# Kernel optimization log

Measured on AMD Instinct MI355X. Metric: run time of the kernel, lower is better.

The kernel has to match this reference:

```python
import jax, jax.numpy as jnp
import numpy as np

jax.config.update("jax_enable_x64", True)

B, N, M_EQ, D_INEQ = 64, 128, 32, 64
RHO = 1.0
THRES = 1e-5
MAX_ITERS = 5000  # safety cap (original loops until relative objective change <= 1e-5)


def setup_inputs() -> dict:
    key = jax.random.key(0)
    kL, kq, kG, kA, kx0, ks = jax.random.split(key, 6)
    L = jax.random.normal(kL, (B, N, N))
    Q = jnp.einsum('bij,bkj->bik', L, L) / N + jnp.eye(N)  # SPD, well-conditioned
    q = jax.random.normal(kq, (B, N))
    G = jax.random.normal(kG, (B, D_INEQ, N))
    A = jax.random.normal(kA, (B, M_EQ, N))
    x0 = jax.random.normal(kx0, (B, N))
    slack = jax.random.uniform(ks, (B, D_INEQ)) + 0.1
    h = jnp.einsum('bdn,bn->bd', G, x0) + slack  # strictly feasible ineq
    b = jnp.einsum('bmn,bn->bm', A, x0)          # feasible eq
    f32 = jnp.float32
    return {"Q": Q.astype(f32), "q": q.astype(f32), "G": G.astype(f32),
            "h": h.astype(f32), "A": A.astype(f32), "b": b.astype(f32)}


def _alt_diff_batch(Q, q, G, h, A, b):
    """Batched Alt-Diff ADMM QP solve; returns (x [B,n], dx/dq [B,n,n])."""
    Bb, n = q.shape
    d = h.shape[1]
    m = b.shape[1]
    dt = Q.dtype
    AtA = jnp.einsum('bmi,bmj->bij', A, A)
    GtG = jnp.einsum('bdi,bdj->bij', G, G)
    R = -jnp.linalg.inv(Q + RHO * AtA + RHO * GtG)
    ATb = RHO * jnp.einsum('bmn,bm->bn', A, b)
    GTh = RHO * jnp.einsum('bdn,bd->bn', G, h)
    eye = jnp.eye(n, dtype=dt)

    def obj(x):
        return 0.5 * jnp.einsum('bi,bij,bj->b', x, Q, x) + jnp.einsum('bi,bi->b', q, x)

    init = dict(
        xk=jnp.zeros((Bb, n), dt), sk=jnp.zeros((Bb, d), dt),
        lamb=jnp.zeros((Bb, m), dt), nu=jnp.zeros((Bb, d), dt),
        dxk=jnp.zeros((Bb, n, n), dt), dsk=jnp.zeros((Bb, d, n), dt),
        dlamb=jnp.zeros((Bb, m, n), dt), dnu=jnp.zeros((Bb, d, n), dt),
        res_prev=jnp.full((Bb,), 1000.0, dt),   # res = [1000, -100] init
        res_cur=jnp.full((Bb,), -100.0, dt),
        done=jnp.zeros((Bb,), bool),
        it=jnp.zeros((), jnp.int32),
    )

    def cond(s):
        return jnp.logical_and(jnp.any(~s["done"]), s["it"] < MAX_ITERS)

    def body(s):
        xk = jnp.einsum('bij,bj->bi', R,
                        q + jnp.einsum('bmn,bm->bn', A, s["lamb"])
                          + jnp.einsum('bdn,bd->bn', G, s["nu"]) - ATb
                          + RHO * jnp.einsum('bdn,bd->bn', G, s["sk"]) - GTh)
        dxk = jnp.einsum('bij,bjk->bik', R,
                         eye + jnp.einsum('bmn,bmk->bnk', A, s["dlamb"])
                             + jnp.einsum('bdn,bdk->bnk', G, s["dnu"])
                             + RHO * jnp.einsum('bdn,bdk->bnk', G, s["dsk"]))
        Gx = jnp.einsum('bdn,bn->bd', G, xk)
        sk = jax.nn.relu(-(1.0 / RHO) * s["nu"] - (Gx - h))
        sgn = (sk > 0).astype(dt)  # sgn applied to already-relu'd sk, as in source
        dsk = (-1.0 / RHO) * sgn[:, :, None] * (s["dnu"] + RHO * jnp.einsum('bdn,bnk->bdk', G, dxk))
        lamb = s["lamb"] + RHO * (jnp.einsum('bmn,bn->bm', A, xk) - b)
        dlamb = s["dlamb"] + RHO * jnp.einsum('bmn,bnk->bmk', A, dxk)
        nu = s["nu"] + RHO * (Gx + sk - h)
        dnu = s["dnu"] + RHO * (jnp.einsum('bdn,bnk->bdk', G, dxk) + dsk)
        res_new = obj(xk)

        keep = s["done"]

        def sel(old, new):
            mask = keep.reshape((-1,) + (1,) * (new.ndim - 1))
            return jnp.where(mask, old, new)

        res_prev = jnp.where(keep, s["res_prev"], s["res_cur"])
        res_cur = jnp.where(keep, s["res_cur"], res_new)
        done = keep | (jnp.abs((res_cur - res_prev) / res_prev) <= THRES)
        return dict(
            xk=sel(s["xk"], xk), sk=sel(s["sk"], sk),
            lamb=sel(s["lamb"], lamb), nu=sel(s["nu"], nu),
            dxk=sel(s["dxk"], dxk), dsk=sel(s["dsk"], dsk),
            dlamb=sel(s["dlamb"], dlamb), dnu=sel(s["dnu"], dnu),
            res_prev=res_prev, res_cur=res_cur, done=done, it=s["it"] + 1,
        )

    final = jax.lax.while_loop(cond, body, init)
    return final["xk"], final["dxk"]


def reference(Q, q, G, h, A, b):
    out_dtype = q.dtype
    f64 = jnp.float64
    x, _dx = _alt_diff_batch(Q.astype(f64), q.astype(f64), G.astype(f64),
                             h.astype(f64), A.astype(f64), b.astype(f64))
    return x.astype(out_dtype)
```

## Files before the change

kernel.cpp:

```cpp
#include <hip/hip_runtime.h>

#define NN 128
#define ME 32
#define DI 64
#define NZ 96
#define ROWD 130
#define MAXIT 5000

#define OFF_UN 16640
#define ROWB  (OFF_UN)
#define COLB  (OFF_UN + 256)
#define PPK   (OFF_UN)
#define ZEXL  (OFF_UN + 384)
#define ZEXH  (OFF_UN + 512)
#define TVX   (OFF_UN + 576)
#define TV16  (OFF_UN + 704)
#define FLG   (OFF_UN + 736)
#define YBUF  (OFF_UN)
#define KBUF  (OFF_UN + 1536)
#define CPART (OFF_UN + 1024)
#define VP    (OFF_UN + 1280)
#define BASEV (OFF_UN + 1792)
#define QBV   (OFF_UN + 1888)
#define FPART (OFF_UN + 1024)
#define RHSV  (OFF_UN + 1280)
#define XPART (OFF_UN + 1408)
#define CB    (OFF_UN + 2688)
#define QBUF  (OFF_UN + 2816)
#define V1    (OFF_UN + 2944)
#define V2    (OFF_UN + 3072)
#define HB    (OFF_UN + 3200)
#define BB    (OFF_UN + 3264)
#define CST   (OFF_UN + 3296)
#define ZBF   (OFF_UN + 3304)
#define LDS_DBL (OFF_UN + 3400)

typedef __attribute__((ext_vector_type(2))) float f32x2;

__device__ __forceinline__ float rlf(float v, int lane) {
  return __uint_as_float((unsigned)__builtin_amdgcn_readlane((int)__float_as_uint(v), lane));
}
__device__ __forceinline__ f32x2 fma2(f32x2 a, f32x2 b, f32x2 c) {
  return __builtin_elementwise_fma(a, b, c);
}

#define MV2(PA, ZS, L0) {                                                  \
    f32x2 z0 = { rlf(ZS, L0), rlf(ZS, (L0)+1) };                           \
    A0 = fma2(Kp[PA], z0, A0); B0 = fma2(Kp2[PA], z0, B0);                 \
    f32x2 z1 = { rlf(ZS, (L0)+2), rlf(ZS, (L0)+3) };                       \
    A1 = fma2(Kp[(PA)+1], z1, A1); B1 = fma2(Kp2[(PA)+1], z1, B1); }

#define CPYRANGE(LBASE, KBASE, CNT)                                        \
  _Pragma("unroll") for (int j = 0; j < (CNT); ++j) {                      \
    const int lj = (LBASE) + j, kc = (KBASE) + j;                          \
    float va = (float)ldsd[KBUF + kc*NZ + l];                              \
    float vb = (float)ldsd[KBUF + kc*NZ + 64 + lm];                        \
    if ((lj & 1) == 0) { Kp[lj>>1].x = va; Kp2[lj>>1].x = vb; }            \
    else               { Kp[lj>>1].y = va; Kp2[lj>>1].y = vb; }            \
  }

__global__ __launch_bounds__(256, 1) void altdiff_kernel(
    const float* __restrict__ Qg, const float* __restrict__ qg,
    const float* __restrict__ Gg, const float* __restrict__ hg,
    const float* __restrict__ Ag, const float* __restrict__ bg,
    float* __restrict__ out)
{
  extern __shared__ double ldsd[];

  const int bidx = blockIdx.x;
  const int tid  = threadIdx.x;
  const int w    = tid >> 6;
  const int l    = tid & 63;
  const int lm   = l & 31;
  const int ia   = tid & 127;
  const int hh   = tid >> 7;

  const float* Qb = Qg + (size_t)bidx * NN * NN;
  const float* Ab = Ag + (size_t)bidx * ME * NN;
  const float* Gb = Gg + (size_t)bidx * DI * NN;
  const float* qb = qg + (size_t)bidx * NN;
  const float* hb = hg + (size_t)bidx * DI;
  const float* bv = bg + (size_t)bidx * ME;

  if (tid < DI) ldsd[HB + tid] = (double)hb[tid];
  else if (tid < DI + ME) ldsd[BB + tid - DI] = (double)bv[tid - DI];
  if (tid >= 128) ldsd[QBUF + tid - 128] = (double)qb[tid - 128];

  const int r = tid >> 4, c = tid & 15;
  double acc[8][8];

  {
    const float4* Q4 = (const float4*)Qb;
#pragma unroll
    for (int rr = 0; rr < 8; ++rr) {
      float4 q0 = Q4[((8*r+rr) << 5) + 2*c];
      float4 q1 = Q4[((8*r+rr) << 5) + 2*c + 1];
      acc[rr][0]=(double)q0.x; acc[rr][1]=(double)q0.y; acc[rr][2]=(double)q0.z; acc[rr][3]=(double)q0.w;
      acc[rr][4]=(double)q1.x; acc[rr][5]=(double)q1.y; acc[rr][6]=(double)q1.z; acc[rr][7]=(double)q1.w;
    }
    const float4* A4 = (const float4*)Ab;
    for (int m = 0; m < ME; ++m) {
      float4 u0 = A4[(m << 5) + 2*r], u1 = A4[(m << 5) + 2*r + 1];
      float4 v0 = A4[(m << 5) + 2*c], v1 = A4[(m << 5) + 2*c + 1];
      double uu[8] = {(double)u0.x,(double)u0.y,(double)u0.z,(double)u0.w,
                      (double)u1.x,(double)u1.y,(double)u1.z,(double)u1.w};
      double vv[8] = {(double)v0.x,(double)v0.y,(double)v0.z,(double)v0.w,
                      (double)v1.x,(double)v1.y,(double)v1.z,(double)v1.w};
#pragma unroll
      for (int rr = 0; rr < 8; ++rr)
#pragma unroll
        for (int cc = 0; cc < 8; ++cc)
          acc[rr][cc] = fma(uu[rr], vv[cc], acc[rr][cc]);
    }
    const float4* G4 = (const float4*)Gb;
    for (int d = 0; d < DI; ++d) {
      float4 u0 = G4[(d << 5) + 2*r], u1 = G4[(d << 5) + 2*r + 1];
      float4 v0 = G4[(d << 5) + 2*c], v1 = G4[(d << 5) + 2*c + 1];
      double uu[8] = {(double)u0.x,(double)u0.y,(double)u0.z,(double)u0.w,
                      (double)u1.x,(double)u1.y,(double)u1.z,(double)u1.w};
      double vv[8] = {(double)v0.x,(double)v0.y,(double)v0.z,(double)v0.w,
                      (double)v1.x,(double)v1.y,(double)v1.z,(double)v1.w};
#pragma unroll
      for (int rr = 0; rr < 8; ++rr)
#pragma unroll
        for (int cc = 0; cc < 8; ++cc)
          acc[rr][cc] = fma(uu[rr], vv[cc], acc[rr][cc]);
    }
  }

  {
    if (r == 0) {
#pragma unroll
      for (int cc = 0; cc < 8; ++cc) ldsd[ROWB + 8*c + cc] = acc[0][cc];
    }
    if (c == 0) {
#pragma unroll
      for (int rr = 0; rr < 8; ++rr) ldsd[COLB + 8*r + rr] = acc[rr][0];
    }
    __syncthreads();
    for (int k = 0; k < NN; ++k) {
      const int pb = (k & 1) << 7;
      const int krt = k >> 3, kcl = k & 7;
      double rowk[8], colv[8];
#pragma unroll
      for (int cc = 0; cc < 8; ++cc) rowk[cc] = ldsd[ROWB + pb + 8*c + cc];
#pragma unroll
      for (int rr = 0; rr < 8; ++rr) colv[rr] = ldsd[COLB + pb + 8*r + rr];
      const double dkk  = ldsd[ROWB + pb + k];
      const double rcpd = 1.0 / dkk;
      double rdv[8];
#pragma unroll
      for (int cc = 0; cc < 8; ++cc) rdv[cc] = rowk[cc] * rcpd;
      const bool pivR = (r == krt), pivC = (c == krt);
#pragma unroll
      for (int rr = 0; rr < 8; ++rr) {
        const double cv = colv[rr] * rcpd;
        const bool pr = pivR && (rr == kcl);
#pragma unroll
        for (int cc = 0; cc < 8; ++cc) {
          double gen = fma(-cv, rowk[cc], acc[rr][cc]);
          acc[rr][cc] = pr ? rdv[cc] : gen;
        }
      }
      if (pivC) {
#pragma unroll
        for (int cc = 0; cc < 8; ++cc) if (cc == kcl) {
#pragma unroll
          for (int rr = 0; rr < 8; ++rr) {
            const bool pr2 = pivR && (rr == kcl);
            acc[rr][cc] = pr2 ? -rcpd : colv[rr] * rcpd;
          }
        }
      }
      if (k < NN - 1) {
        const int pb2 = ((k + 1) & 1) << 7;
        const int krt2 = (k + 1) >> 3, kcl2 = (k + 1) & 7;
        if (r == krt2) {
#pragma unroll
          for (int rr = 0; rr < 8; ++rr) if (rr == kcl2) {
#pragma unroll
            for (int cc = 0; cc < 8; ++cc) ldsd[ROWB + pb2 + 8*c + cc] = acc[rr][cc];
          }
        }
        if (c == krt2) {
#pragma unroll
          for (int cc = 0; cc < 8; ++cc) if (cc == kcl2) {
#pragma unroll
            for (int rr = 0; rr < 8; ++rr) ldsd[COLB + pb2 + 8*r + rr] = acc[rr][cc];
          }
        }
      }
      __syncthreads();
    }
#pragma unroll
    for (int rr = 0; rr < 8; ++rr) {
      double2* dst = (double2*)(ldsd + (8*r+rr)*ROWD + 8*c);
#pragma unroll
      for (int t = 0; t < 4; ++t) dst[t] = make_double2(acc[rr][2*t], acc[rr][2*t+1]);
    }
  }
  __syncthreads();

  f32x2 Kp[16], Kp2[16];
  for (int blk = 0; blk < 8; ++blk) {
    {
      const float* gp[6];
#pragma unroll
      for (int jj = 0; jj < 6; ++jj) {
        int it = 12*blk + 6*hh + jj;
        gp[jj] = (it < DI) ? (Gb + it*NN) : (Ab + (it - DI)*NN);
      }
      double a2[6] = {0,0,0,0,0,0};
#pragma unroll 4
      for (int t = 0; t < NN; ++t) {
        double rv = ldsd[t*ROWD + ia];
#pragma unroll
        for (int jj = 0; jj < 6; ++jj)
          a2[jj] = fma(rv, (double)gp[jj][t], a2[jj]);
      }
      double2* yst = (double2*)(ldsd + YBUF + ia*12 + 6*hh);
#pragma unroll
      for (int p = 0; p < 3; ++p) yst[p] = make_double2(a2[2*p], a2[2*p+1]);
    }
    __syncthreads();
    {
      const int r2 = (ia < NZ) ? ia : 0;
      const float* brow = (r2 < DI) ? (Gb + r2*NN) : (Ab + (r2 - DI)*NN);
      double a2[6] = {0,0,0,0,0,0};
#pragma unroll 4
      for (int t = 0; t < NN; ++t) {
        double bvv = (double)brow[t];
        const double2* yr = (const double2*)(ldsd + YBUF + t*12 + 6*hh);
        double2 y0 = yr[0], y1 = yr[1], y2 = yr[2];
        a2[0] = fma(bvv, y0.x, a2[0]); a2[1] = fma(bvv, y0.y, a2[1]);
        a2[2] = fma(bvv, y1.x, a2[2]); a2[3] = fma(bvv, y1.y, a2[3]);
        a2[4] = fma(bvv, y2.x, a2[4]); a2[5] = fma(bvv, y2.y, a2[5]);
      }
      if (ia < NZ) {
#pragma unroll
        for (int jj = 0; jj < 6; ++jj) ldsd[KBUF + (6*hh + jj)*NZ + ia] = a2[jj];
      }
    }
    __syncthreads();
    if (w == 0) {
      if (blk == 0)      { CPYRANGE(0,  0, 12) }
      else if (blk == 1) { CPYRANGE(12, 0, 12) }
      else if (blk == 2) { CPYRANGE(24, 0, 8) }
    } else if (w == 1) {
      if (blk == 2)      { CPYRANGE(0,  8, 4) }
      else if (blk == 3) { CPYRANGE(4,  0, 12) }
      else if (blk == 4) { CPYRANGE(16, 0, 12) }
      else if (blk == 5) { CPYRANGE(28, 0, 4) }
    } else if (w == 2) {
      if (blk == 5)      { CPYRANGE(0,  4, 8) }
      else if (blk == 6) { CPYRANGE(8,  0, 12) }
      else if (blk == 7) { CPYRANGE(20, 0, 12) }
    }
    __syncthreads();
  }

  {
    double s = 0;
#pragma unroll 8
    for (int jc = 0; jc < 48; ++jc) {
      int j = 48*hh + jc;
      double coef = (j < DI) ? ldsd[HB + j] : ldsd[BB + j - DI];
      const float* src = (j < DI) ? (Gb + j*NN) : (Ab + (j - DI)*NN);
      s = fma(-(double)src[ia], coef, s);
    }
    ldsd[CPART + hh*128 + ia] = s;
  }
  __syncthreads();
  if (tid < NN) ldsd[CB + tid] = ldsd[QBUF + tid] + ldsd[CPART + tid] + ldsd[CPART + 128 + tid];
  __syncthreads();

  {
    double a = 0, b2 = 0;
#pragma unroll 4
    for (int tt = 0; tt < 64; ++tt) {
      int t = 64*hh + tt;
      double rv = ldsd[t*ROWD + ia];
      a  = fma(rv, ldsd[CB + t], a);
      b2 = fma(rv, ldsd[QBUF + t], b2);
    }
    ldsd[VP + hh*128 + ia] = a;
    ldsd[VP + 256 + hh*128 + ia] = b2;
  }
  __syncthreads();
  if (tid < NN) {
    ldsd[V1 + tid] = ldsd[VP + tid] + ldsd[VP + 128 + tid];
    ldsd[V2 + tid] = ldsd[VP + 256 + tid] + ldsd[VP + 384 + tid];
  }
  __syncthreads();

  {
    const int r2 = (ia < NZ) ? ia : 0;
    const float* brow = (r2 < DI) ? (Gb + r2*NN) : (Ab + (r2 - DI)*NN);
    const int voff = hh ? V2 : V1;
    double s = 0;
#pragma unroll 4
    for (int t = 0; t < NN; ++t) s = fma((double)brow[t], ldsd[voff + t], s);
    if (ia < NZ) ldsd[(hh ? QBV : BASEV) + ia] = s;
  }
  if (w == 0) {
    double pc = ldsd[V1+l]*ldsd[CB+l]   + ldsd[V1+64+l]*ldsd[CB+64+l];
    double pq = ldsd[V1+l]*ldsd[QBUF+l] + ldsd[V1+64+l]*ldsd[QBUF+64+l];
#pragma unroll
    for (int off = 32; off >= 1; off >>= 1) { pc += __shfl_xor(pc, off); pq += __shfl_xor(pq, off); }
    if (l == 0) { ldsd[CST] = pc; ldsd[CST+1] = pq; }
  }
  __syncthreads();

  const double baseA = ldsd[BASEV + l];
  const double baseB = ldsd[BASEV + 64 + lm];
  const double qvA   = ldsd[QBV + l];
  const double qvB   = ldsd[QBV + 64 + lm];
  const double hb2   = ldsd[HB + l] - baseA;
  const double bb2   = baseB - ldsd[BB + lm];
  const double S_uc  = ldsd[CST], S_qu = ldsd[CST + 1];
  double hnb = hb2, lb = bb2;
  double zlo = 0.0, zhi = 0.0;
  double zAlo = 0.0, zAhi = 0.0, zBlo = 0.0, zBhi = 0.0, zClo = 0.0, zChi = 0.0;
  double res_prev = 1000.0, res_cur = -100.0;
  float2 own = make_float2(0.f, 0.f);

  {
    if (w < 3) *(float2*)&ldsd[PPK + w*64 + l] = make_float2(0.f, 0.f);
    if (w == 0) ldsd[ZEXL + 64 + l] = 0.0;
    if (w == 2 && l < 32) ldsd[ZEXH + 32 + l] = 0.0;
    if (tid == 0) { ldsd[FLG] = 0.0; ldsd[FLG + 1] = 0.0; }
  }

  for (int it = 0; it < MAXIT + 3; ++it) {
    __syncthreads();
    const int buf = it & 1, nbuf = buf ^ 1;
    const int bprev = nbuf;
    const double fl = ldsd[FLG + bprev];
    const float2* pb = (const float2*)(ldsd + PPK + buf*192);

    if (w == 0) {
      float2 s1v = pb[64 + l], s2v = pb[128 + l];
      float slo = (own.x + s1v.x) + s2v.x;
      double t = hnb - (double)slo;
      float zflo = (float)fabs(t);
      if (it >= 3 && fl != 0.0) break;
      zClo = zBlo; zBlo = zAlo; zAlo = zlo;
      if (it < MAXIT) {
        zlo = fabs(t);
        ldsd[ZEXL + buf*64 + l] = zlo;
        hnb = hb2 + fmin(t, 0.0);
        f32x2 A0 = {0.f, 0.f}, A1 = A0, B0 = A0, B1 = A0;
        MV2(0,  zflo, 0)  MV2(2,  zflo, 4)  MV2(4,  zflo, 8)  MV2(6,  zflo, 12)
        MV2(8,  zflo, 16) MV2(10, zflo, 20) MV2(12, zflo, 24) MV2(14, zflo, 28)
        f32x2 As = A0 + A1, Bs = B0 + B1;
        float2 np = make_float2(As.x + As.y, Bs.x + Bs.y);
        *(float2*)&ldsd[PPK + nbuf*192 + l] = np;
        own = np;
      }
    } else if (w == 1) {
      float2 s0v = pb[l], s2v = pb[128 + l];
      float slo = (s0v.x + own.x) + s2v.x;
      double t = hnb - (double)slo;
      float zflo = (float)fabs(t);
      if (it >= 3 && fl != 0.0) break;
      if (it < MAXIT) {
        hnb = hb2 + fmin(t, 0.0);
        f32x2 A0 = {0.f, 0.f}, A1 = A0, B0 = A0, B1 = A0;
        MV2(0,  zflo, 32) MV2(2,  zflo, 36) MV2(4,  zflo, 40) MV2(6,  zflo, 44)
        MV2(8,  zflo, 48) MV2(10, zflo, 52) MV2(12, zflo, 56) MV2(14, zflo, 60)
        f32x2 As = A0 + A1, Bs = B0 + B1;
        float2 np = make_float2(As.x + As.y, Bs.x + Bs.y);
        *(float2*)&ldsd[PPK + nbuf*192 + 64 + l] = np;
        own = np;
      }
    } else if (w == 2) {
      float2 s0v = pb[l], s1v = pb[64 + l];
      float shi = (s0v.y + s1v.y) + own.y;
      double lamn = lb + (double)shi;
      float zfhi = (float)lamn;
      if (it >= 3 && fl != 0.0) break;
      zChi = zBhi; zBhi = zAhi; zAhi = zhi;
      if (it < MAXIT) {
        zhi = lamn;
        lb = lamn + bb2;
        if (l < 32) ldsd[ZEXH + buf*32 + l] = lamn;
        f32x2 A0 = {0.f, 0.f}, A1 = A0, B0 = A0, B1 = A0;
        MV2(0,  zfhi, 0)  MV2(2,  zfhi, 4)  MV2(4,  zfhi, 8)  MV2(6,  zfhi, 12)
        MV2(8,  zfhi, 16) MV2(10, zfhi, 20) MV2(12, zfhi, 24) MV2(14, zfhi, 28)
        f32x2 As = A0 + A1, Bs = B0 + B1;
        float2 np = make_float2(As.x + As.y, Bs.x + Bs.y);
        *(float2*)&ldsd[PPK + nbuf*192 + 128 + l] = np;
        own = np;
      }
    } else {
      float2 v0 = pb[l], v1 = pb[64 + l], v2 = pb[128 + l];
      const double zAl = ldsd[ZEXL + bprev*64 + l];
      const double zAh = ldsd[ZEXH + bprev*32 + lm];
      const int g = l & 15;
      const double* tq = ldsd + TVX + bprev*64;
      double a0 = tq[g], a1 = tq[g + 16], a2 = tq[g + 32], a3 = tq[g + 48];
      double t1v[16];
      const double2* tp = (const double2*)(ldsd + TV16 + bprev*16);
#pragma unroll
      for (int u = 0; u < 8; ++u) { double2 vv = tp[u]; t1v[2*u] = vv.x; t1v[2*u+1] = vv.y; }
      if (it >= 3 && fl != 0.0) break;
      if (it < MAXIT) {
        float slo_f = (v0.x + v1.x) + v2.x;
        float shi_f = (v0.y + v1.y) + v2.y;
        double yf  = (double)slo_f + baseA;
        double tvl = fma(qvA, zAl, -0.5*(zAl*(baseA + yf) + yf*yf));
        double yfB = (double)shi_f + baseB;
        double tvh = fma(qvB, zAh, -0.5*(zAh*(baseB + yfB) + yfB*yfB));
        ldsd[TVX + buf*64 + l] = tvl + ((l < 32) ? tvh : 0.0);
      }
      if (l < 16 && it >= 1 && it <= MAXIT)
        ldsd[TV16 + buf*16 + l] = (a0 + a1) + (a2 + a3);
      if (it >= 2 && it <= MAXIT + 1) {
        double s1 = ((t1v[0] + t1v[1]) + (t1v[2] + t1v[3])) + ((t1v[4] + t1v[5]) + (t1v[6] + t1v[7]));
        double s2 = ((t1v[8] + t1v[9]) + (t1v[10] + t1v[11])) + ((t1v[12] + t1v[13]) + (t1v[14] + t1v[15]));
        double obj = (s1 + s2) - 0.5*S_uc + S_qu;
        res_prev = res_cur; res_cur = obj;
        if (l == 0)
          ldsd[FLG + buf] = (fabs(res_cur - res_prev) <= 1e-5 * fabs(res_prev)) ? 1.0 : 0.0;
      }
    }
  }

  if (w == 0) ldsd[ZBF + l] = zClo;
  if (w == 2 && l < 32) ldsd[ZBF + 64 + l] = zChi;
  __syncthreads();
  {
    double s = 0;
#pragma unroll 8
    for (int jc = 0; jc < 48; ++jc) {
      int j = 48*hh + jc;
      double zj = ldsd[ZBF + j];
      const float* src = (j < DI) ? (Gb + j*NN) : (Ab + (j - DI)*NN);
      s = fma((double)src[ia], zj, s);
    }
    ldsd[FPART + hh*128 + ia] = s;
  }
  __syncthreads();
  if (tid < NN) ldsd[RHSV + tid] = ldsd[CB + tid] + ldsd[FPART + tid] + ldsd[FPART + 128 + tid];
  __syncthreads();
  {
    double s = 0;
#pragma unroll 4
    for (int tt = 0; tt < 64; ++tt) {
      int t = 64*hh + tt;
      s = fma(ldsd[t*ROWD + ia], ldsd[RHSV + t], s);
    }
    ldsd[XPART + hh*128 + ia] = s;
  }
  __syncthreads();
  if (tid < NN)
    out[(size_t)bidx * NN + tid] = (float)(ldsd[XPART + tid] + ldsd[XPART + 128 + tid]);
}

extern "C" void kernel_launch(void* const* d_in, const int* in_sizes, int n_in,
                              void* d_out, int out_size, void* d_ws, size_t ws_size,
                              hipStream_t stream) {
  (void)in_sizes; (void)n_in; (void)out_size; (void)d_ws; (void)ws_size;
  const float* Q = (const float*)d_in[0];
  const float* q = (const float*)d_in[1];
  const float* G = (const float*)d_in[2];
  const float* h = (const float*)d_in[3];
  const float* A = (const float*)d_in[4];
  const float* b = (const float*)d_in[5];
  float* out = (float*)d_out;
  const size_t lds_bytes = (size_t)LDS_DBL * sizeof(double);
  altdiff_kernel<<<dim3(64), dim3(256), lds_bytes, stream>>>(Q, q, G, h, A, b, out);
}
```

Baseline: 598.7 us.

## Spread ADMM matvec across all four waves and track iterates in float

Rebalances the per-iteration ADMM matvec so all four wavefronts each own 28/28/24/16 rows of the packed K matrix, rather than three waves doing the matvec while the fourth only evaluates the objective. Each wave now reads all four partial-sum slots and redundantly recomputes the z/lambda update, which removes the ZEXL/ZEXH exchange buffers. The history of iterates is kept in float instead of double. This shortens the matvec on the critical path per iteration, but adds an extra partial to read and sum, and the float history could change the convergence check and the final reconstruction.

```diff
diff --git a/kernel.cpp b/kernel.cpp
--- a/kernel.cpp
+++ b/kernel.cpp
@@ -11,11 +11,9 @@
 #define ROWB  (OFF_UN)
 #define COLB  (OFF_UN + 256)
 #define PPK   (OFF_UN)
-#define ZEXL  (OFF_UN + 384)
-#define ZEXH  (OFF_UN + 512)
-#define TVX   (OFF_UN + 576)
-#define TV16  (OFF_UN + 704)
-#define FLG   (OFF_UN + 736)
+#define TVX   (OFF_UN + 512)
+#define TV16  (OFF_UN + 640)
+#define FLG   (OFF_UN + 672)
 #define YBUF  (OFF_UN)
 #define KBUF  (OFF_UN + 1536)
 #define CPART (OFF_UN + 1024)
@@ -201,7 +199,7 @@
   }
   __syncthreads();
 
-  f32x2 Kp[16], Kp2[16];
+  f32x2 Kp[14], Kp2[14];
   for (int blk = 0; blk < 8; ++blk) {
     {
       const float* gp[6];
@@ -245,16 +243,18 @@
     if (w == 0) {
       if (blk == 0)      { CPYRANGE(0,  0, 12) }
       else if (blk == 1) { CPYRANGE(12, 0, 12) }
-      else if (blk == 2) { CPYRANGE(24, 0, 8) }
+      else if (blk == 2) { CPYRANGE(24, 0, 4) }
     } else if (w == 1) {
-      if (blk == 2)      { CPYRANGE(0,  8, 4) }
-      else if (blk == 3) { CPYRANGE(4,  0, 12) }
-      else if (blk == 4) { CPYRANGE(16, 0, 12) }
-      else if (blk == 5) { CPYRANGE(28, 0, 4) }
+      if (blk == 2)      { CPYRANGE(0,  4, 8) }
+      else if (blk == 3) { CPYRANGE(8,  0, 12) }
+      else if (blk == 4) { CPYRANGE(20, 0, 8) }
     } else if (w == 2) {
-      if (blk == 5)      { CPYRANGE(0,  4, 8) }
-      else if (blk == 6) { CPYRANGE(8,  0, 12) }
-      else if (blk == 7) { CPYRANGE(20, 0, 12) }
+      if (blk == 4)      { CPYRANGE(0,  8, 4) }
+      else if (blk == 5) { CPYRANGE(4,  0, 12) }
+      else if (blk == 6) { CPYRANGE(16, 0, 8) }
+    } else {
+      if (blk == 6)      { CPYRANGE(0,  8, 4) }
+      else if (blk == 7) { CPYRANGE(4,  0, 12) }
     }
     __syncthreads();
   }
@@ -319,15 +319,13 @@
   const double bb2   = baseB - ldsd[BB + lm];
   const double S_uc  = ldsd[CST], S_qu = ldsd[CST + 1];
   double hnb = hb2, lb = bb2;
-  double zlo = 0.0, zhi = 0.0;
-  double zAlo = 0.0, zAhi = 0.0, zBlo = 0.0, zBhi = 0.0, zClo = 0.0, zChi = 0.0;
+  float hnbf = (float)hnb, lbf = (float)lb;
+  float zplo = 0.f, zphi = 0.f;
+  float zAlo = 0.f, zAhi = 0.f, zBlo = 0.f, zBhi = 0.f, zClo = 0.f, zChi = 0.f;
   double res_prev = 1000.0, res_cur = -100.0;
-  float2 own = make_float2(0.f, 0.f);
-
-  {
-    if (w < 3) *(float2*)&ldsd[PPK + w*64 + l] = make_float2(0.f, 0.f);
-    if (w == 0) ldsd[ZEXL + 64 + l] = 0.0;
-    if (w == 2 && l < 32) ldsd[ZEXH + 32 + l] = 0.0;
+
+  {
+    *(float2*)&ldsd[PPK + w*64 + l] = make_float2(0.f, 0.f);
     if (tid == 0) { ldsd[FLG] = 0.0; ldsd[FLG + 1] = 0.0; }
   }
 
@@ -336,83 +334,64 @@
     const int buf = it & 1, nbuf = buf ^ 1;
     const int bprev = nbuf;
     const double fl = ldsd[FLG + bprev];
-    const float2* pb = (const float2*)(ldsd + PPK + buf*192);
-
-    if (w == 0) {
-      float2 s1v = pb[64 + l], s2v = pb[128 + l];
-      float slo = (own.x + s1v.x) + s2v.x;
-      double t = hnb - (double)slo;
-      float zflo = (float)fabs(t);
-      if (it >= 3 && fl != 0.0) break;
-      zClo = zBlo; zBlo = zAlo; zAlo = zlo;
-      if (it < MAXIT) {
-        zlo = fabs(t);
-        ldsd[ZEXL + buf*64 + l] = zlo;
-        hnb = hb2 + fmin(t, 0.0);
-        f32x2 A0 = {0.f, 0.f}, A1 = A0, B0 = A0, B1 = A0;
-        MV2(0,  zflo, 0)  MV2(2,  zflo, 4)  MV2(4,  zflo, 8)  MV2(6,  zflo, 12)
-        MV2(8,  zflo, 16) MV2(10, zflo, 20) MV2(12, zflo, 24) MV2(14, zflo, 28)
-        f32x2 As = A0 + A1, Bs = B0 + B1;
-        float2 np = make_float2(As.x + As.y, Bs.x + Bs.y);
-        *(float2*)&ldsd[PPK + nbuf*192 + l] = np;
-        own = np;
-      }
-    } else if (w == 1) {
-      float2 s0v = pb[l], s2v = pb[128 + l];
-      float slo = (s0v.x + own.x) + s2v.x;
-      double t = hnb - (double)slo;
-      float zflo = (float)fabs(t);
-      if (it >= 3 && fl != 0.0) break;
-      if (it < MAXIT) {
-        hnb = hb2 + fmin(t, 0.0);
-        f32x2 A0 = {0.f, 0.f}, A1 = A0, B0 = A0, B1 = A0;
-        MV2(0,  zflo, 32) MV2(2,  zflo, 36) MV2(4,  zflo, 40) MV2(6,  zflo, 44)
-        MV2(8,  zflo, 48) MV2(10, zflo, 52) MV2(12, zflo, 56) MV2(14, zflo, 60)
-        f32x2 As = A0 + A1, Bs = B0 + B1;
-        float2 np = make_float2(As.x + As.y, Bs.x + Bs.y);
-        *(float2*)&ldsd[PPK + nbuf*192 + 64 + l] = np;
-        own = np;
-      }
-    } else if (w == 2) {
-      float2 s0v = pb[l], s1v = pb[64 + l];
-      float shi = (s0v.y + s1v.y) + own.y;
-      double lamn = lb + (double)shi;
-      float zfhi = (float)lamn;
-      if (it >= 3 && fl != 0.0) break;
-      zChi = zBhi; zBhi = zAhi; zAhi = zhi;
-      if (it < MAXIT) {
-        zhi = lamn;
-        lb = lamn + bb2;
-        if (l < 32) ldsd[ZEXH + buf*32 + l] = lamn;
-        f32x2 A0 = {0.f, 0.f}, A1 = A0, B0 = A0, B1 = A0;
-        MV2(0,  zfhi, 0)  MV2(2,  zfhi, 4)  MV2(4,  zfhi, 8)  MV2(6,  zfhi, 12)
-        MV2(8,  zfhi, 16) MV2(10, zfhi, 20) MV2(12, zfhi, 24) MV2(14, zfhi, 28)
-        f32x2 As = A0 + A1, Bs = B0 + B1;
-        float2 np = make_float2(As.x + As.y, Bs.x + Bs.y);
-        *(float2*)&ldsd[PPK + nbuf*192 + 128 + l] = np;
-        own = np;
-      }
-    } else {
-      float2 v0 = pb[l], v1 = pb[64 + l], v2 = pb[128 + l];
-      const double zAl = ldsd[ZEXL + bprev*64 + l];
-      const double zAh = ldsd[ZEXH + bprev*32 + lm];
+    const float2* pb = (const float2*)(ldsd + PPK + buf*256);
+    float2 p0 = pb[l], p1 = pb[64 + l], p2 = pb[128 + l], p3 = pb[192 + l];
+    double a0 = 0, a1 = 0, a2 = 0, a3 = 0;
+    double t1v[16];
+    if (w == 3) {
       const int g = l & 15;
       const double* tq = ldsd + TVX + bprev*64;
-      double a0 = tq[g], a1 = tq[g + 16], a2 = tq[g + 32], a3 = tq[g + 48];
-      double t1v[16];
+      a0 = tq[g]; a1 = tq[g + 16]; a2 = tq[g + 32]; a3 = tq[g + 48];
       const double2* tp = (const double2*)(ldsd + TV16 + bprev*16);
 #pragma unroll
       for (int u = 0; u < 8; ++u) { double2 vv = tp[u]; t1v[2*u] = vv.x; t1v[2*u+1] = vv.y; }
-      if (it >= 3 && fl != 0.0) break;
-      if (it < MAXIT) {
-        float slo_f = (v0.x + v1.x) + v2.x;
-        float shi_f = (v0.y + v1.y) + v2.y;
-        double yf  = (double)slo_f + baseA;
+    }
+    float slo = (p0.x + p1.x) + (p2.x + p3.x);
+    float tf   = hnbf - slo;
+    float zflo = fabsf(tf);
+    float shi = 0.f, zfhi = 0.f;
+    if (w >= 2) {
+      shi  = (p0.y + p1.y) + (p2.y + p3.y);
+      zfhi = lbf + shi;
+    }
+    if (it >= 3 && fl != 0.0) break;
+    if (w == 3) { zClo = zBlo; zChi = zBhi; zBlo = zAlo; zBhi = zAhi; zAlo = zplo; zAhi = zphi; }
+    if (it < MAXIT) {
+      double t = hnb - (double)slo;
+      hnb = hb2 + fmin(t, 0.0);
+      hnbf = (float)hnb;
+      if (w >= 2) {
+        double lamn = lb + (double)shi;
+        lb = lamn + bb2;
+        lbf = (float)lb;
+      }
+      if (w == 3) { zplo = zflo; zphi = zfhi; }
+      f32x2 A0 = {0.f, 0.f}, A1 = A0, B0 = A0, B1 = A0;
+      if (w == 0) {
+        MV2(0,  zflo, 0)  MV2(2,  zflo, 4)  MV2(4,  zflo, 8)  MV2(6,  zflo, 12)
+        MV2(8,  zflo, 16) MV2(10, zflo, 20) MV2(12, zflo, 24)
+      } else if (w == 1) {
+        MV2(0,  zflo, 28) MV2(2,  zflo, 32) MV2(4,  zflo, 36) MV2(6,  zflo, 40)
+        MV2(8,  zflo, 44) MV2(10, zflo, 48) MV2(12, zflo, 52)
+      } else if (w == 2) {
+        MV2(0,  zflo, 56) MV2(2,  zflo, 60)
+        MV2(4,  zfhi, 0)  MV2(6,  zfhi, 4)  MV2(8,  zfhi, 8)  MV2(10, zfhi, 12)
+      } else {
+        MV2(0,  zfhi, 16) MV2(2,  zfhi, 20) MV2(4,  zfhi, 24) MV2(6,  zfhi, 28)
+      }
+      f32x2 As = A0 + A1, Bs = B0 + B1;
+      *(float2*)&ldsd[PPK + nbuf*256 + w*64 + l] = make_float2(As.x + As.y, Bs.x + Bs.y);
+      if (w == 3) {
+        double yf  = (double)slo + baseA;
+        double zAl = (double)zAlo;
         double tvl = fma(qvA, zAl, -0.5*(zAl*(baseA + yf) + yf*yf));
-        double yfB = (double)shi_f + baseB;
+        double yfB = (double)shi + baseB;
+        double zAh = (double)zAhi;
         double tvh = fma(qvB, zAh, -0.5*(zAh*(baseB + yfB) + yfB*yfB));
         ldsd[TVX + buf*64 + l] = tvl + ((l < 32) ? tvh : 0.0);
       }
+    }
+    if (w == 3) {
       if (l < 16 && it >= 1 && it <= MAXIT)
         ldsd[TV16 + buf*16 + l] = (a0 + a1) + (a2 + a3);
       if (it >= 2 && it <= MAXIT + 1) {
@@ -426,8 +405,10 @@
     }
   }
 
-  if (w == 0) ldsd[ZBF + l] = zClo;
-  if (w == 2 && l < 32) ldsd[ZBF + 64 + l] = zChi;
+  if (w == 3) {
+    ldsd[ZBF + l] = (double)zClo;
+    if (l < 32) ldsd[ZBF + 64 + l] = (double)zChi;
+  }
   __syncthreads();
   {
     double s = 0;
```

After: 685.9 us. 1.15x slower.
